# Optimization experiments

Hardware: AMD Instinct MI355X
Metric: run time of the kernel (lower is better)

The kernel has to match this reference:

```python
import jax, jax.numpy as jnp
import numpy as np
from jax import lax

B, T, C = 64, 1024, 512
INIT_P = 1.0
CLAMP_LO, CLAMP_HI = 1e-4, 1.0 - 1e-4


def setup_inputs() -> dict:
    key = jax.random.key(0)
    k1, k2 = jax.random.split(key)
    x = jax.random.normal(k1, (B, T, C), dtype=jnp.float32)
    # learnable per-channel logit(lambda); original inits to logit(0.98) repeated,
    # use randn around that value so gradients are nontrivial
    init_logit = float(np.log(0.98 / (1.0 - 0.98)))
    logit_lambda = init_logit + 0.1 * jax.random.normal(k2, (C,), dtype=jnp.float32)
    return {"x": x, "logit_lambda": logit_lambda}


def reference(x, logit_lambda):
    # lam: [C] -> broadcast over (B, C) states
    lam = jnp.clip(jax.nn.sigmoid(logit_lambda), CLAMP_LO, CLAMP_HI)
    theta0 = x[:, 0, :]                                   # [B, C]
    P0 = jnp.full(theta0.shape, INIT_P, dtype=x.dtype)    # [B, C]

    def step(carry, xt):
        theta, P = carry
        K = P / (lam + P)                 # gain, data-independent of x
        theta = theta + K * (xt - theta)  # level update
        P = (P - K * P) / lam             # covariance update
        return (theta, P), theta

    xs = jnp.swapaxes(x, 0, 1)[1:]        # [T-1, B, C], timesteps 1..T-1
    _, ys = lax.scan(step, (theta0, P0), xs)
    # y[:,0,:] = x[:,0,:], y[:,t,:] = theta_t for t>=1
    y = jnp.concatenate([theta0[:, None, :], jnp.swapaxes(ys, 0, 1)], axis=1)
    return y
```

## Files before the change

kernel.cpp:

```cpp
#include <hip/hip_runtime.h>
#include <math.h>


namespace {
constexpr int kB = 64;
constexpr int kT = 1024;
constexpr int kC = 512;
constexpr int kNCH = 16;
constexpr int kL = kT / kNCH;
constexpr int kCV = kC / 4;
}

__device__ __forceinline__ void load_lam(const float* __restrict__ zl, int c0,
                                         float lam[4]) {
  float4 z = *reinterpret_cast<const float4*>(zl + c0);
  float zz[4] = {z.x, z.y, z.z, z.w};
#pragma unroll
  for (int k = 0; k < 4; ++k) {
    float s = 1.0f / (1.0f + expf(-zz[k]));
    lam[k] = fminf(fmaxf(s, 1e-4f), 1.0f - 1e-4f);
  }
}

extern "C" __global__ __launch_bounds__(256) void ewrls_carry(
    const float* __restrict__ x, const float* __restrict__ zl,
    float4* __restrict__ carry) {
  int idx = blockIdx.x * 256 + threadIdx.x;
  int cv = idx % kCV;
  int bj = idx / kCV;
  int j = bj % (kNCH - 1);
  int b = bj / (kNCH - 1);
  float lam[4];
  load_lam(zl, cv * 4, lam);

  const float4* xp = reinterpret_cast<const float4*>(x) +
                     ((size_t)b * kT + (size_t)j * kL) * kCV + cv;
  float s0 = 0.f, s1 = 0.f, s2 = 0.f, s3 = 0.f;
#pragma unroll 4
  for (int t = 0; t < kL; ++t) {
    float4 v = xp[(size_t)t * kCV];
    s0 = fmaf(lam[0], s0, v.x);
    s1 = fmaf(lam[1], s1, v.y);
    s2 = fmaf(lam[2], s2, v.z);
    s3 = fmaf(lam[3], s3, v.w);
  }
  carry[((size_t)b * kNCH + j) * kCV + cv] = make_float4(s0, s1, s2, s3);
}

extern "C" __global__ __launch_bounds__(256) void ewrls_out(
    const float* __restrict__ x, const float* __restrict__ zl,
    const float4* __restrict__ carry, float* __restrict__ y) {
  int idx = blockIdx.x * 256 + threadIdx.x;
  int cv = idx % kCV;
  int bj = idx / kCV;
  int j = bj % kNCH;
  int b = bj / kNCH;
  float lam[4];
  load_lam(zl, cv * 4, lam);

  float lamL[4];
#pragma unroll
  for (int k = 0; k < 4; ++k) {
    float p = lam[k];
#pragma unroll
    for (int q = 0; q < 6; ++q) p = p * p;
    lamL[k] = p;
  }

  float S[4] = {0.f, 0.f, 0.f, 0.f};
  float pj[4] = {1.f, 1.f, 1.f, 1.f};
  for (int i = 0; i < j; ++i) {
    float4 cr = carry[((size_t)b * kNCH + i) * kCV + cv];
    S[0] = fmaf(lamL[0], S[0], cr.x);
    S[1] = fmaf(lamL[1], S[1], cr.y);
    S[2] = fmaf(lamL[2], S[2], cr.z);
    S[3] = fmaf(lamL[3], S[3], cr.w);
    pj[0] *= lamL[0];
    pj[1] *= lamL[1];
    pj[2] *= lamL[2];
    pj[3] *= lamL[3];
  }

  float Q[4];
#pragma unroll
  for (int k = 0; k < 4; ++k) Q[k] = (1.0f - pj[k]) / (1.0f - lam[k]);

  const size_t base = ((size_t)b * kT + (size_t)j * kL) * kCV + cv;
  const float4* xp = reinterpret_cast<const float4*>(x) + base;
  float4* yp = reinterpret_cast<float4*>(y) + base;
#pragma unroll 4
  for (int t = 0; t < kL; ++t) {
    float4 v = xp[(size_t)t * kCV];
    S[0] = fmaf(lam[0], S[0], v.x);
    S[1] = fmaf(lam[1], S[1], v.y);
    S[2] = fmaf(lam[2], S[2], v.z);
    S[3] = fmaf(lam[3], S[3], v.w);
    Q[0] = fmaf(lam[0], Q[0], 1.0f);
    Q[1] = fmaf(lam[1], Q[1], 1.0f);
    Q[2] = fmaf(lam[2], Q[2], 1.0f);
    Q[3] = fmaf(lam[3], Q[3], 1.0f);
    float4 o;
    o.x = S[0] / Q[0];
    o.y = S[1] / Q[1];
    o.z = S[2] / Q[2];
    o.w = S[3] / Q[3];
    yp[(size_t)t * kCV] = o;
  }
}

extern "C" __global__ __launch_bounds__(256) void ewrls_serial(
    const float* __restrict__ x, const float* __restrict__ zl,
    float* __restrict__ y) {
  int idx = blockIdx.x * 256 + threadIdx.x;
  int cv = idx % kCV;
  int b = idx / kCV;
  float lam[4];
  load_lam(zl, cv * 4, lam);
  float S[4] = {0.f, 0.f, 0.f, 0.f};
  float Q[4] = {0.f, 0.f, 0.f, 0.f};
  const size_t base = (size_t)b * kT * kCV + cv;
  const float4* xp = reinterpret_cast<const float4*>(x) + base;
  float4* yp = reinterpret_cast<float4*>(y) + base;
#pragma unroll 4
  for (int t = 0; t < kT; ++t) {
    float4 v = xp[(size_t)t * kCV];
    S[0] = fmaf(lam[0], S[0], v.x);
    S[1] = fmaf(lam[1], S[1], v.y);
    S[2] = fmaf(lam[2], S[2], v.z);
    S[3] = fmaf(lam[3], S[3], v.w);
    Q[0] = fmaf(lam[0], Q[0], 1.0f);
    Q[1] = fmaf(lam[1], Q[1], 1.0f);
    Q[2] = fmaf(lam[2], Q[2], 1.0f);
    Q[3] = fmaf(lam[3], Q[3], 1.0f);
    float4 o;
    o.x = S[0] / Q[0];
    o.y = S[1] / Q[1];
    o.z = S[2] / Q[2];
    o.w = S[3] / Q[3];
    yp[(size_t)t * kCV] = o;
  }
}

extern "C" void kernel_launch(void* const* d_in, const int* in_sizes, int n_in,
                              void* d_out, int out_size, void* d_ws,
                              size_t ws_size, hipStream_t stream) {
  const float* x = (const float*)d_in[0];
  const float* zl = (const float*)d_in[1];
  float* y = (float*)d_out;

  const size_t need = (size_t)kB * kNCH * kCV * sizeof(float4);
  if (ws_size >= need) {
    float4* carry = (float4*)d_ws;
    const int n1 = kB * (kNCH - 1) * kCV;
    ewrls_carry<<<n1 / 256, 256, 0, stream>>>(x, zl, carry);
    const int n2 = kB * kNCH * kCV;
    ewrls_out<<<n2 / 256, 256, 0, stream>>>(x, zl, carry, y);
  } else {
    const int n = kB * kCV;
    ewrls_serial<<<n / 256, 256, 0, stream>>>(x, zl, y);
  }
}
```

Before: 263.9 us.

## Double chunk count, use fast reciprocal, nontemporal IO, deeper unroll in EWRLS scan

Splits the time axis into 32 chunks instead of 16, doubling parallelism in both the carry and output passes, and adjusts the chunk decay power to lambda^32. It replaces the IEEE divisions with the hardware approximate reciprocal, uses nontemporal loads and stores for the streaming x/y traffic, and raises the loop unroll factor to 8. More chunks lengthen the sequential carry-combine loop and add carry traffic, and the approximate reciprocal may slightly change accuracy.

```diff
diff --git a/kernel.cpp b/kernel.cpp
--- a/kernel.cpp
+++ b/kernel.cpp
@@ -6,25 +6,26 @@
 constexpr int kB = 64;
 constexpr int kT = 1024;
 constexpr int kC = 512;
-constexpr int kNCH = 16;
+constexpr int kNCH = 32;
 constexpr int kL = kT / kNCH;
 constexpr int kCV = kC / 4;
 }
 
+typedef float vfloat4 __attribute__((ext_vector_type(4)));
+
 __device__ __forceinline__ void load_lam(const float* __restrict__ zl, int c0,
                                          float lam[4]) {
-  float4 z = *reinterpret_cast<const float4*>(zl + c0);
-  float zz[4] = {z.x, z.y, z.z, z.w};
+  vfloat4 z = *reinterpret_cast<const vfloat4*>(zl + c0);
 #pragma unroll
   for (int k = 0; k < 4; ++k) {
-    float s = 1.0f / (1.0f + expf(-zz[k]));
+    float s = 1.0f / (1.0f + expf(-z[k]));
     lam[k] = fminf(fmaxf(s, 1e-4f), 1.0f - 1e-4f);
   }
 }
 
 extern "C" __global__ __launch_bounds__(256) void ewrls_carry(
     const float* __restrict__ x, const float* __restrict__ zl,
-    float4* __restrict__ carry) {
+    vfloat4* __restrict__ carry) {
   int idx = blockIdx.x * 256 + threadIdx.x;
   int cv = idx % kCV;
   int bj = idx / kCV;
@@ -33,23 +34,24 @@
   float lam[4];
   load_lam(zl, cv * 4, lam);
 
-  const float4* xp = reinterpret_cast<const float4*>(x) +
-                     ((size_t)b * kT + (size_t)j * kL) * kCV + cv;
+  const vfloat4* xp = reinterpret_cast<const vfloat4*>(x) +
+                      ((size_t)b * kT + (size_t)j * kL) * kCV + cv;
   float s0 = 0.f, s1 = 0.f, s2 = 0.f, s3 = 0.f;
-#pragma unroll 4
+#pragma unroll 8
   for (int t = 0; t < kL; ++t) {
-    float4 v = xp[(size_t)t * kCV];
+    vfloat4 v = xp[(size_t)t * kCV];
     s0 = fmaf(lam[0], s0, v.x);
     s1 = fmaf(lam[1], s1, v.y);
     s2 = fmaf(lam[2], s2, v.z);
     s3 = fmaf(lam[3], s3, v.w);
   }
-  carry[((size_t)b * kNCH + j) * kCV + cv] = make_float4(s0, s1, s2, s3);
+  vfloat4 cr = {s0, s1, s2, s3};
+  carry[((size_t)b * kNCH + j) * kCV + cv] = cr;
 }
 
 extern "C" __global__ __launch_bounds__(256) void ewrls_out(
     const float* __restrict__ x, const float* __restrict__ zl,
-    const float4* __restrict__ carry, float* __restrict__ y) {
+    const vfloat4* __restrict__ carry, float* __restrict__ y) {
   int idx = blockIdx.x * 256 + threadIdx.x;
   int cv = idx % kCV;
   int bj = idx / kCV;
@@ -63,14 +65,14 @@
   for (int k = 0; k < 4; ++k) {
     float p = lam[k];
 #pragma unroll
-    for (int q = 0; q < 6; ++q) p = p * p;
+    for (int q = 0; q < 5; ++q) p = p * p;
     lamL[k] = p;
   }
 
   float S[4] = {0.f, 0.f, 0.f, 0.f};
   float pj[4] = {1.f, 1.f, 1.f, 1.f};
   for (int i = 0; i < j; ++i) {
-    float4 cr = carry[((size_t)b * kNCH + i) * kCV + cv];
+    vfloat4 cr = carry[((size_t)b * kNCH + i) * kCV + cv];
     S[0] = fmaf(lamL[0], S[0], cr.x);
     S[1] = fmaf(lamL[1], S[1], cr.y);
     S[2] = fmaf(lamL[2], S[2], cr.z);
@@ -83,14 +85,15 @@
 
   float Q[4];
 #pragma unroll
-  for (int k = 0; k < 4; ++k) Q[k] = (1.0f - pj[k]) / (1.0f - lam[k]);
+  for (int k = 0; k < 4; ++k)
+    Q[k] = (1.0f - pj[k]) * __builtin_amdgcn_rcpf(1.0f - lam[k]);
 
   const size_t base = ((size_t)b * kT + (size_t)j * kL) * kCV + cv;
-  const float4* xp = reinterpret_cast<const float4*>(x) + base;
-  float4* yp = reinterpret_cast<float4*>(y) + base;
-#pragma unroll 4
+  const vfloat4* xp = reinterpret_cast<const vfloat4*>(x) + base;
+  vfloat4* yp = reinterpret_cast<vfloat4*>(y) + base;
+#pragma unroll 8
   for (int t = 0; t < kL; ++t) {
-    float4 v = xp[(size_t)t * kCV];
+    vfloat4 v = __builtin_nontemporal_load(&xp[(size_t)t * kCV]);
     S[0] = fmaf(lam[0], S[0], v.x);
     S[1] = fmaf(lam[1], S[1], v.y);
     S[2] = fmaf(lam[2], S[2], v.z);
@@ -99,12 +102,12 @@
     Q[1] = fmaf(lam[1], Q[1], 1.0f);
     Q[2] = fmaf(lam[2], Q[2], 1.0f);
     Q[3] = fmaf(lam[3], Q[3], 1.0f);
-    float4 o;
-    o.x = S[0] / Q[0];
-    o.y = S[1] / Q[1];
-    o.z = S[2] / Q[2];
-    o.w = S[3] / Q[3];
-    yp[(size_t)t * kCV] = o;
+    vfloat4 o;
+    o.x = S[0] * __builtin_amdgcn_rcpf(Q[0]);
+    o.y = S[1] * __builtin_amdgcn_rcpf(Q[1]);
+    o.z = S[2] * __builtin_amdgcn_rcpf(Q[2]);
+    o.w = S[3] * __builtin_amdgcn_rcpf(Q[3]);
+    __builtin_nontemporal_store(o, &yp[(size_t)t * kCV]);
   }
 }
 
@@ -119,11 +122,11 @@
   float S[4] = {0.f, 0.f, 0.f, 0.f};
   float Q[4] = {0.f, 0.f, 0.f, 0.f};
   const size_t base = (size_t)b * kT * kCV + cv;
-  const float4* xp = reinterpret_cast<const float4*>(x) + base;
-  float4* yp = reinterpret_cast<float4*>(y) + base;
+  const vfloat4* xp = reinterpret_cast<const vfloat4*>(x) + base;
+  vfloat4* yp = reinterpret_cast<vfloat4*>(y) + base;
 #pragma unroll 4
   for (int t = 0; t < kT; ++t) {
-    float4 v = xp[(size_t)t * kCV];
+    vfloat4 v = xp[(size_t)t * kCV];
     S[0] = fmaf(lam[0], S[0], v.x);
     S[1] = fmaf(lam[1], S[1], v.y);
     S[2] = fmaf(lam[2], S[2], v.z);
@@ -132,11 +135,11 @@
     Q[1] = fmaf(lam[1], Q[1], 1.0f);
     Q[2] = fmaf(lam[2], Q[2], 1.0f);
     Q[3] = fmaf(lam[3], Q[3], 1.0f);
-    float4 o;
-    o.x = S[0] / Q[0];
-    o.y = S[1] / Q[1];
-    o.z = S[2] / Q[2];
-    o.w = S[3] / Q[3];
+    vfloat4 o;
+    o.x = S[0] * __builtin_amdgcn_rcpf(Q[0]);
+    o.y = S[1] * __builtin_amdgcn_rcpf(Q[1]);
+    o.z = S[2] * __builtin_amdgcn_rcpf(Q[2]);
+    o.w = S[3] * __builtin_amdgcn_rcpf(Q[3]);
     yp[(size_t)t * kCV] = o;
   }
 }
@@ -148,9 +151,9 @@
   const float* zl = (const float*)d_in[1];
   float* y = (float*)d_out;
 
-  const size_t need = (size_t)kB * kNCH * kCV * sizeof(float4);
+  const size_t need = (size_t)kB * kNCH * kCV * sizeof(vfloat4);
   if (ws_size >= need) {
-    float4* carry = (float4*)d_ws;
+    vfloat4* carry = (vfloat4*)d_ws;
     const int n1 = kB * (kNCH - 1) * kCV;
     ewrls_carry<<<n1 / 256, 256, 0, stream>>>(x, zl, carry);
     const int n2 = kB * kNCH * kCV;
```

Measured after the change: 260.8 us. Within noise of the previous version (-1.2%).
